# Kernel optimization log

Hardware: AMD Instinct MI355X
Metric: run time of the kernel (lower is better)

## Reference

```python
import jax, jax.numpy as jnp
import numpy as np

SEQ, BATCH, INP = 20, 16384, 2
HID, EMB = 256, 64
TARGET_LEN = 30


def setup_inputs() -> dict:
    key = jax.random.key(0)
    ks = jax.random.split(key, 12)
    s = 0.1
    return {
        "x_input": jax.random.normal(ks[0], (SEQ, BATCH, INP), dtype=jnp.float32),
        # encoder embedding Linear(input_size -> emb_dim)
        "W_emb": jax.random.normal(ks[1], (EMB, INP), dtype=jnp.float32) * s,
        "b_emb": jax.random.normal(ks[2], (EMB,), dtype=jnp.float32) * s,
        # encoder LSTM (input EMB -> hidden HID), PyTorch gate order i,f,g,o; bias = b_ih + b_hh
        "W_ih_enc": jax.random.normal(ks[3], (4 * HID, EMB), dtype=jnp.float32) * s,
        "W_hh_enc": jax.random.normal(ks[4], (4 * HID, HID), dtype=jnp.float32) * s,
        "b_enc": jax.random.normal(ks[5], (4 * HID,), dtype=jnp.float32) * s,
        # decoder LSTM (input INP -> hidden HID)
        "W_ih_dec": jax.random.normal(ks[6], (4 * HID, INP), dtype=jnp.float32) * s,
        "W_hh_dec": jax.random.normal(ks[7], (4 * HID, HID), dtype=jnp.float32) * s,
        "b_dec": jax.random.normal(ks[8], (4 * HID,), dtype=jnp.float32) * s,
        # decoder output Linear(hidden -> input_size)
        "W_out": jax.random.normal(ks[9], (INP, HID), dtype=jnp.float32) * s,
        "b_out": jax.random.normal(ks[10], (INP,), dtype=jnp.float32) * s,
        "target_len": TARGET_LEN,
    }


def _lstm_cell(x, h, c, W_ih, W_hh, b):
    # x: [B, in], h/c: [B, H]; PyTorch gate order: input, forget, cell(g), output
    gates = x @ W_ih.T + h @ W_hh.T + b  # [B, 4H]
    i, f, g, o = jnp.split(gates, 4, axis=-1)
    c_new = jax.nn.sigmoid(f) * c + jax.nn.sigmoid(i) * jnp.tanh(g)
    h_new = jax.nn.sigmoid(o) * jnp.tanh(c_new)
    return h_new, c_new


def reference(x_input, W_emb, b_emb, W_ih_enc, W_hh_enc, b_enc,
              W_ih_dec, W_hh_dec, b_dec, W_out, b_out, target_len):
    B = x_input.shape[1]
    # --- encoder ---
    x_emb = x_input @ W_emb.T + b_emb  # [S, B, EMB]
    h0 = jnp.zeros((B, HID), dtype=x_input.dtype)
    c0 = jnp.zeros((B, HID), dtype=x_input.dtype)

    def enc_step(carry, xt):
        h, c = carry
        h, c = _lstm_cell(xt, h, c, W_ih_enc, W_hh_enc, b_enc)
        return (h, c), None

    (h_enc, c_enc), _ = jax.lax.scan(enc_step, (h0, c0), x_emb)

    dec_in0 = x_input[-1]  # [B, INP]

    def dec_step(carry, _):
        di, h, c = carry
        h, c = _lstm_cell(di, h, c, W_ih_dec, W_hh_dec, b_dec)
        out = h @ W_out.T + b_out  # [B, INP]
        return (out, h, c), out

    _, outputs = jax.lax.scan(dec_step, (dec_in0, h_enc, c_enc), None,
                              length=int(target_len))
    return outputs  # [target_len, B, INP]
```

## Files before the change

kernel.cpp:

```cpp
#include <hip/hip_runtime.h>


#define SEQ  20
#define TLEN 30
#define LOG2E  1.442695041f
#define LOG2E2 2.885390082f

typedef _Float16 half8   __attribute__((ext_vector_type(8)));
typedef _Float16 half4   __attribute__((ext_vector_type(4)));
typedef _Float16 half2v  __attribute__((ext_vector_type(2)));
typedef float    floatx4 __attribute__((ext_vector_type(4)));

__device__ _Float16 g_w_enc[1024 * 288];
__device__ _Float16 g_w_dec0[1024 * 288];
__device__ _Float16 g_w_deff[1024 * 288];
__device__ _Float16 g_wout[512];

__global__ void prep_kernel(const float* __restrict__ W_emb,
                            const float* __restrict__ b_emb,
                            const float* __restrict__ W_ih_enc,
                            const float* __restrict__ W_hh_enc,
                            const float* __restrict__ b_enc,
                            const float* __restrict__ W_ih_dec,
                            const float* __restrict__ W_hh_dec,
                            const float* __restrict__ b_dec,
                            const float* __restrict__ W_out,
                            const float* __restrict__ b_out) {
    int gid = blockIdx.x * blockDim.x + threadIdx.x;
    int stride = gridDim.x * blockDim.x;
    for (int s = gid; s < 1024 * 288; s += stride) {
        int n = s / 288, k = s - n * 288;
        int g = n >> 8, c = (n >> 4) & 15, l16 = n & 15;
        int w = c >> 1, cc = c & 1;
        int i = cc * 4 + g;
        int kt = k >> 5, q = (k >> 3) & 3, j = k & 7;
        int dst = ((w * 9 + kt) * 8 + i) * 512 + q * 128 + l16 * 8 + j;
        float sc = (g == 2) ? LOG2E2 : LOG2E;
        float fe = 0.f, fd = 0.f, ff = 0.f;
        if (k < 256) {
            fe = W_hh_enc[n * 256 + k];
            fd = W_hh_dec[n * 256 + k];
            ff = fd + W_ih_dec[2 * n] * W_out[k]
                    + W_ih_dec[2 * n + 1] * W_out[256 + k];
        } else {
            int kp = k - 256;
            if (kp < 2) {
                fd = W_ih_dec[2 * n + kp];
                const float* wr = &W_ih_enc[n * 64];
                for (int e = 0; e < 64; e++) fe = fmaf(wr[e], W_emb[2 * e + kp], fe);
            } else if (kp == 2) {
                fd = b_dec[n];
                ff = b_dec[n] + W_ih_dec[2 * n] * b_out[0]
                              + W_ih_dec[2 * n + 1] * b_out[1];
                fe = b_enc[n];
                const float* wr = &W_ih_enc[n * 64];
                for (int e = 0; e < 64; e++) fe = fmaf(wr[e], b_emb[e], fe);
            }
        }
        g_w_enc[dst]  = (_Float16)(fe * sc);
        g_w_dec0[dst] = (_Float16)(fd * sc);
        g_w_deff[dst] = (_Float16)(ff * sc);
    }
    if (gid < 512) g_wout[gid] = (_Float16)W_out[gid];
}

__global__ __launch_bounds__(512, 2) void lstm_fused(
        const float* __restrict__ x_input,
        const float* __restrict__ b_out,
        float* __restrict__ out)
{
    __shared__ __align__(16) _Float16 h_pack[2][18432];
    __shared__ __align__(16) float    partial_lds[2][8 * 132];
    __shared__ int flag_lds[9];
    __shared__ int cnt_lds[2];

    const int tid = threadIdx.x;
    const int w   = tid >> 6;
    const int L   = tid & 63;
    const int l16 = L & 15;
    const int q   = L >> 4;
    const long row0 = (long)blockIdx.x * 64;

    {
        int* hz = (int*)&h_pack[0][0];
        for (int idx = tid; idx < 18432; idx += 512) hz[idx] = 0;
        if (tid < 9) flag_lds[tid] = 0;
        if (tid < 2) cnt_lds[tid] = 0;
    }
    __syncthreads();
    if (tid < 128) {
        int buf = tid >> 6, b = tid & 63;
        h_pack[buf][((b >> 4) * 9 + 8) * 512 + (b & 15) * 8 + 2] = (_Float16)1.f;
    }
    if (tid < 128) {
        int b = tid >> 1, jj = tid & 1;
        h_pack[0][((b >> 4) * 9 + 8) * 512 + (b & 15) * 8 + jj] =
            (_Float16)x_input[(row0 + b) * 2 + jj];
    }

    const float2 bo2 = make_float2(b_out[0], b_out[1]);
    const int aoff = q * 128 + l16 * 8;
    const _Float16* __restrict__ wenc_w  = &g_w_enc[w * 36864];
    const _Float16* __restrict__ wdec0_w = &g_w_dec0[w * 36864];
    const _Float16* __restrict__ wdeff_w = &g_w_deff[w * 36864];

    _Float16 wo[2][2][4];
#pragma unroll
    for (int jj = 0; jj < 2; jj++)
#pragma unroll
        for (int cc = 0; cc < 2; cc++)
#pragma unroll
            for (int r = 0; r < 4; r++)
                wo[jj][cc][r] = g_wout[jj * 256 + 32 * w + 16 * cc + 4 * q + r];

    floatx4 acc[8][4];
    float   c_st[4][2][4];
#pragma unroll
    for (int nt = 0; nt < 4; nt++)
#pragma unroll
        for (int cc = 0; cc < 2; cc++)
#pragma unroll
            for (int r = 0; r < 4; r++) c_st[nt][cc][r] = 0.f;

    __syncthreads();

    auto flag_ld = [&](int idx) {
        return __hip_atomic_load(&flag_lds[idx], __ATOMIC_RELAXED,
                                 __HIP_MEMORY_SCOPE_WORKGROUP);
    };

#pragma unroll 1
    for (int t = 0; t < SEQ + TLEN; t++) {
        const _Float16* __restrict__ Wb =
            (t < SEQ) ? wenc_w : (t == SEQ) ? wdec0_w : wdeff_w;
        const _Float16* __restrict__ hp = h_pack[t & 1];
        _Float16* __restrict__ hn = h_pack[(t + 1) & 1];

        int pf = flag_ld(0);
#pragma unroll
        for (int kt = 0; kt < 9; kt++) {
            int pfn = 0;
            if (kt < 8) pfn = flag_ld(kt + 1);
            while (pf < t) {
                __builtin_amdgcn_s_sleep(1);
                pf = flag_ld(kt);
            }
            __builtin_amdgcn_sched_barrier(0);
            half8 B[4];
#pragma unroll
            for (int nt = 0; nt < 4; nt++)
                B[nt] = *(const half8*)&hp[(nt * 9 + kt) * 512 + aoff];
#pragma unroll
            for (int i = 0; i < 8; i++) {
                half8 Aw = *(const half8*)&Wb[(kt * 8 + i) * 512 + aoff];
                if (kt == 0) {
#pragma unroll
                    for (int nt = 0; nt < 4; nt++)
                        acc[i][nt] = __builtin_amdgcn_mfma_f32_16x16x32_f16(
                            Aw, B[nt], (floatx4)(0.f), 0, 0, 0);
                } else {
#pragma unroll
                    for (int nt = 0; nt < 4; nt++)
                        acc[i][nt] = __builtin_amdgcn_mfma_f32_16x16x32_f16(
                            Aw, B[nt], acc[i][nt], 0, 0, 0);
                }
            }
            pf = pfn;
        }

        float2 xv2 = make_float2(0.f, 0.f);
        if (w == 0 && t < SEQ) {
            int srct = (t + 1 < SEQ) ? t + 1 : SEQ - 1;
            xv2 = *(const float2*)&x_input[(long)srct * 32768 + (row0 + L) * 2];
        }

        const bool dec = (t >= SEQ);
        const int par = t & 1;
        float po[4][2];
#pragma unroll
        for (int nt = 0; nt < 4; nt++) { po[nt][0] = 0.f; po[nt][1] = 0.f; }

#pragma unroll
        for (int nt = 0; nt < 4; nt++)
#pragma unroll
            for (int cc = 0; cc < 2; cc++) {
                half4 hv4;
                float hvf[4];
#pragma unroll
                for (int r = 0; r < 4; r++) {
                    float ai = acc[cc * 4 + 0][nt][r];
                    float af = acc[cc * 4 + 1][nt][r];
                    float ag = acc[cc * 4 + 2][nt][r];
                    float ao = acc[cc * 4 + 3][nt][r];
                    float eI = __builtin_amdgcn_exp2f(-ai);
                    float eG = __builtin_amdgcn_exp2f(-ag);
                    float eF = __builtin_amdgcn_exp2f(-af);
                    float eO = __builtin_amdgcn_exp2f(-ao);
                    float ig = (1.f - eG) *
                        __builtin_amdgcn_rcpf((1.f + eI) * (1.f + eG));
                    float fs = __builtin_amdgcn_rcpf(1.f + eF);
                    float cn = fmaf(fs, c_st[nt][cc][r], ig);
                    c_st[nt][cc][r] = cn;
                    float cnc = fminf(fmaxf(cn, -12.f), 12.f);
                    float eC = __builtin_amdgcn_exp2f(-LOG2E2 * cnc);
                    float hv = (1.f - eC) *
                        __builtin_amdgcn_rcpf((1.f + eO) * (1.f + eC));
                    hvf[r] = hv;
                    hv4[r] = (_Float16)hv;
                }
                *(half4*)&hn[(nt * 9 + w) * 512 + (2 * cc + (q >> 1)) * 128 +
                             l16 * 8 + 4 * (q & 1)] = hv4;
                if (dec) {
#pragma unroll
                    for (int r = 0; r < 4; r++) {
                        po[nt][0] = fmaf(hvf[r], (float)wo[0][cc][r], po[nt][0]);
                        po[nt][1] = fmaf(hvf[r], (float)wo[1][cc][r], po[nt][1]);
                    }
                }
            }

        if (L == 0)
            __hip_atomic_store(&flag_lds[w], t + 1, __ATOMIC_RELEASE,
                               __HIP_MEMORY_SCOPE_WORKGROUP);

        if (w == 0) {
            if (t < SEQ) {
                half2v xh; xh[0] = (_Float16)xv2.x; xh[1] = (_Float16)xv2.y;
                *(half2v*)&hn[((L >> 4) * 9 + 8) * 512 + (L & 15) * 8] = xh;
            }
            if (L == 0)
                __hip_atomic_store(&flag_lds[8], t + 1, __ATOMIC_RELEASE,
                                   __HIP_MEMORY_SCOPE_WORKGROUP);
        }

        if (dec) {
#pragma unroll
            for (int nt = 0; nt < 4; nt++)
#pragma unroll
                for (int jj = 0; jj < 2; jj++) {
                    float s = po[nt][jj];
                    s += __shfl_xor(s, 16);
                    s += __shfl_xor(s, 32);
                    po[nt][jj] = s;
                }
            if (q == 0) {
                float* pl = &partial_lds[par][w * 132];
#pragma unroll
                for (int nt = 0; nt < 4; nt++) {
                    pl[nt * 16 + l16]      = po[nt][0];
                    pl[66 + nt * 16 + l16] = po[nt][1];
                }
            }
            __threadfence_block();
            int arr = 0;
            if (L == 0) arr = atomicAdd(&cnt_lds[par], 1);
            arr = __shfl(arr, 0);
            if (arr == 7) {
                if (L == 0)
                    __hip_atomic_store(&cnt_lds[par], 0, __ATOMIC_RELAXED,
                                       __HIP_MEMORY_SCOPE_WORKGROUP);
                float s0 = bo2.x, s1 = bo2.y;
#pragma unroll
                for (int w8 = 0; w8 < 8; w8++) {
                    s0 += partial_lds[par][w8 * 132 + L];
                    s1 += partial_lds[par][w8 * 132 + 66 + L];
                }
                *(float2*)&out[(long)(t - SEQ) * 32768 + (row0 + L) * 2] =
                    make_float2(s0, s1);
            }
        }
    }
}

extern "C" void kernel_launch(void* const* d_in, const int* in_sizes, int n_in,
                              void* d_out, int out_size, void* d_ws, size_t ws_size,
                              hipStream_t stream) {
    (void)in_sizes; (void)n_in; (void)d_ws; (void)ws_size; (void)out_size;
    const float* x      = (const float*)d_in[0];
    const float* W_emb  = (const float*)d_in[1];
    const float* b_emb  = (const float*)d_in[2];
    const float* W_ih_e = (const float*)d_in[3];
    const float* W_hh_e = (const float*)d_in[4];
    const float* b_enc  = (const float*)d_in[5];
    const float* W_ih_d = (const float*)d_in[6];
    const float* W_hh_d = (const float*)d_in[7];
    const float* b_dec  = (const float*)d_in[8];
    const float* W_out  = (const float*)d_in[9];
    const float* b_out  = (const float*)d_in[10];
    float* outp = (float*)d_out;

    prep_kernel<<<512, 256, 0, stream>>>(W_emb, b_emb, W_ih_e, W_hh_e, b_enc,
                                         W_ih_d, W_hh_d, b_dec, W_out, b_out);
    lstm_fused<<<256, 512, 0, stream>>>(x, b_out, outp);
}
```

Measured before the change: 614.2 us.

## Split workgroup into two batch-half groups with paired-wave weight sharing

Rebuilds the work split so that each of two 4-wave groups handles 32 batch rows and each wave computes 64 hidden units (16 gate tiles × 2 batch tiles), where before each wave did 32 hidden units for all 64 rows. Sync changes from per-k-tile flags to per-group hidden-state flags, plus an 'amf' handshake that staggers the two groups so that waves with the same weight slice run in lockstep, presumably to share weight loads through cache. The aim is to cut cross-wave dependency and increase weight reuse per B load. In exchange each wave streams twice as many weight fragments per step, and the new spin-wait coupling adds latency and some deadlock risk.

```diff
diff --git a/kernel.cpp b/kernel.cpp
--- a/kernel.cpp
+++ b/kernel.cpp
@@ -31,10 +31,10 @@
     for (int s = gid; s < 1024 * 288; s += stride) {
         int n = s / 288, k = s - n * 288;
         int g = n >> 8, c = (n >> 4) & 15, l16 = n & 15;
-        int w = c >> 1, cc = c & 1;
+        int wl = c >> 2, cc = c & 3;
         int i = cc * 4 + g;
         int kt = k >> 5, q = (k >> 3) & 3, j = k & 7;
-        int dst = ((w * 9 + kt) * 8 + i) * 512 + q * 128 + l16 * 8 + j;
+        int dst = ((wl * 9 + kt) * 16 + i) * 512 + q * 128 + l16 * 8 + j;
         float sc = (g == 2) ? LOG2E2 : LOG2E;
         float fe = 0.f, fd = 0.f, ff = 0.f;
         if (k < 256) {
@@ -70,12 +70,16 @@
         float* __restrict__ out)
 {
     __shared__ __align__(16) _Float16 h_pack[2][18432];
-    __shared__ __align__(16) float    partial_lds[2][8 * 132];
-    __shared__ int flag_lds[9];
-    __shared__ int cnt_lds[2];
+    __shared__ __align__(16) float    partial_lds[2][2][4 * 68];
+    __shared__ int hflag[2][4];
+    __shared__ int amf[2][4];
+    __shared__ int cnt[2][2];
 
     const int tid = threadIdx.x;
     const int w   = tid >> 6;
+    const int grp = w >> 2;
+    const int wl  = w & 3;
+    const int ntb = grp * 2;
     const int L   = tid & 63;
     const int l16 = L & 15;
     const int q   = L >> 4;
@@ -84,8 +88,9 @@
     {
         int* hz = (int*)&h_pack[0][0];
         for (int idx = tid; idx < 18432; idx += 512) hz[idx] = 0;
-        if (tid < 9) flag_lds[tid] = 0;
-        if (tid < 2) cnt_lds[tid] = 0;
+        if (tid < 8)  hflag[tid >> 2][tid & 3] = 0;
+        if (tid < 16 && tid >= 8) amf[(tid - 8) >> 2][tid & 3] = 0;
+        if (tid < 20 && tid >= 16) cnt[(tid - 16) >> 1][tid & 1] = 0;
     }
     __syncthreads();
     if (tid < 128) {
@@ -98,34 +103,34 @@
             (_Float16)x_input[(row0 + b) * 2 + jj];
     }
 
-    const float2 bo2 = make_float2(b_out[0], b_out[1]);
+    const float boL = b_out[L & 1];
     const int aoff = q * 128 + l16 * 8;
-    const _Float16* __restrict__ wenc_w  = &g_w_enc[w * 36864];
-    const _Float16* __restrict__ wdec0_w = &g_w_dec0[w * 36864];
-    const _Float16* __restrict__ wdeff_w = &g_w_deff[w * 36864];
-
-    _Float16 wo[2][2][4];
+    const _Float16* __restrict__ wenc_w  = &g_w_enc[wl * 73728];
+    const _Float16* __restrict__ wdec0_w = &g_w_dec0[wl * 73728];
+    const _Float16* __restrict__ wdeff_w = &g_w_deff[wl * 73728];
+
+    _Float16 wo[2][4][4];
 #pragma unroll
     for (int jj = 0; jj < 2; jj++)
 #pragma unroll
-        for (int cc = 0; cc < 2; cc++)
+        for (int cc = 0; cc < 4; cc++)
 #pragma unroll
             for (int r = 0; r < 4; r++)
-                wo[jj][cc][r] = g_wout[jj * 256 + 32 * w + 16 * cc + 4 * q + r];
-
-    floatx4 acc[8][4];
-    float   c_st[4][2][4];
-#pragma unroll
-    for (int nt = 0; nt < 4; nt++)
-#pragma unroll
-        for (int cc = 0; cc < 2; cc++)
-#pragma unroll
-            for (int r = 0; r < 4; r++) c_st[nt][cc][r] = 0.f;
+                wo[jj][cc][r] = g_wout[jj * 256 + 64 * wl + 16 * cc + 4 * q + r];
+
+    floatx4 acc[16][2];
+    float   c_st[2][4][4];
+#pragma unroll
+    for (int ntl = 0; ntl < 2; ntl++)
+#pragma unroll
+        for (int cc = 0; cc < 4; cc++)
+#pragma unroll
+            for (int r = 0; r < 4; r++) c_st[ntl][cc][r] = 0.f;
 
     __syncthreads();
 
-    auto flag_ld = [&](int idx) {
-        return __hip_atomic_load(&flag_lds[idx], __ATOMIC_RELAXED,
+    auto ld32 = [&](int* p) {
+        return __hip_atomic_load(p, __ATOMIC_RELAXED,
                                  __HIP_MEMORY_SCOPE_WORKGROUP);
     };
 
@@ -136,62 +141,65 @@
         const _Float16* __restrict__ hp = h_pack[t & 1];
         _Float16* __restrict__ hn = h_pack[(t + 1) & 1];
 
-        int pf = flag_ld(0);
+        if (grp == 1) {
+            while (ld32(&amf[0][wl]) < t + 1) __builtin_amdgcn_s_sleep(1);
+        } else {
+            while (ld32(&amf[1][wl]) < t - 1) __builtin_amdgcn_s_sleep(1);
+        }
+        while (ld32(&hflag[grp][0]) < t || ld32(&hflag[grp][1]) < t ||
+               ld32(&hflag[grp][2]) < t || ld32(&hflag[grp][3]) < t)
+            __builtin_amdgcn_s_sleep(1);
+        __builtin_amdgcn_sched_barrier(0);
+
 #pragma unroll
         for (int kt = 0; kt < 9; kt++) {
-            int pfn = 0;
-            if (kt < 8) pfn = flag_ld(kt + 1);
-            while (pf < t) {
-                __builtin_amdgcn_s_sleep(1);
-                pf = flag_ld(kt);
-            }
-            __builtin_amdgcn_sched_barrier(0);
-            half8 B[4];
-#pragma unroll
-            for (int nt = 0; nt < 4; nt++)
-                B[nt] = *(const half8*)&hp[(nt * 9 + kt) * 512 + aoff];
-#pragma unroll
-            for (int i = 0; i < 8; i++) {
-                half8 Aw = *(const half8*)&Wb[(kt * 8 + i) * 512 + aoff];
+            half8 B0 = *(const half8*)&hp[(ntb * 9 + kt) * 512 + aoff];
+            half8 B1 = *(const half8*)&hp[((ntb + 1) * 9 + kt) * 512 + aoff];
+#pragma unroll
+            for (int i = 0; i < 16; i++) {
+                half8 Aw = *(const half8*)&Wb[(kt * 16 + i) * 512 + aoff];
                 if (kt == 0) {
-#pragma unroll
-                    for (int nt = 0; nt < 4; nt++)
-                        acc[i][nt] = __builtin_amdgcn_mfma_f32_16x16x32_f16(
-                            Aw, B[nt], (floatx4)(0.f), 0, 0, 0);
+                    acc[i][0] = __builtin_amdgcn_mfma_f32_16x16x32_f16(
+                        Aw, B0, (floatx4)(0.f), 0, 0, 0);
+                    acc[i][1] = __builtin_amdgcn_mfma_f32_16x16x32_f16(
+                        Aw, B1, (floatx4)(0.f), 0, 0, 0);
                 } else {
-#pragma unroll
-                    for (int nt = 0; nt < 4; nt++)
-                        acc[i][nt] = __builtin_amdgcn_mfma_f32_16x16x32_f16(
-                            Aw, B[nt], acc[i][nt], 0, 0, 0);
-                }
-            }
-            pf = pfn;
-        }
+                    acc[i][0] = __builtin_amdgcn_mfma_f32_16x16x32_f16(
+                        Aw, B0, acc[i][0], 0, 0, 0);
+                    acc[i][1] = __builtin_amdgcn_mfma_f32_16x16x32_f16(
+                        Aw, B1, acc[i][1], 0, 0, 0);
+                }
+            }
+        }
+
+        if (L == 0)
+            __hip_atomic_store(&amf[grp][wl], t + 1, __ATOMIC_RELAXED,
+                               __HIP_MEMORY_SCOPE_WORKGROUP);
 
         float2 xv2 = make_float2(0.f, 0.f);
-        if (w == 0 && t < SEQ) {
+        if (wl == 0 && t < SEQ && L < 32) {
             int srct = (t + 1 < SEQ) ? t + 1 : SEQ - 1;
-            xv2 = *(const float2*)&x_input[(long)srct * 32768 + (row0 + L) * 2];
+            xv2 = *(const float2*)
+                &x_input[(long)srct * 32768 + (row0 + grp * 32 + L) * 2];
         }
 
         const bool dec = (t >= SEQ);
         const int par = t & 1;
-        float po[4][2];
-#pragma unroll
-        for (int nt = 0; nt < 4; nt++) { po[nt][0] = 0.f; po[nt][1] = 0.f; }
-
-#pragma unroll
-        for (int nt = 0; nt < 4; nt++)
-#pragma unroll
-            for (int cc = 0; cc < 2; cc++) {
+        float po[2][2];
+        po[0][0] = 0.f; po[0][1] = 0.f; po[1][0] = 0.f; po[1][1] = 0.f;
+
+#pragma unroll
+        for (int ntl = 0; ntl < 2; ntl++)
+#pragma unroll
+            for (int cc = 0; cc < 4; cc++) {
                 half4 hv4;
                 float hvf[4];
 #pragma unroll
                 for (int r = 0; r < 4; r++) {
-                    float ai = acc[cc * 4 + 0][nt][r];
-                    float af = acc[cc * 4 + 1][nt][r];
-                    float ag = acc[cc * 4 + 2][nt][r];
-                    float ao = acc[cc * 4 + 3][nt][r];
+                    float ai = acc[cc * 4 + 0][ntl][r];
+                    float af = acc[cc * 4 + 1][ntl][r];
+                    float ag = acc[cc * 4 + 2][ntl][r];
+                    float ao = acc[cc * 4 + 3][ntl][r];
                     float eI = __builtin_amdgcn_exp2f(-ai);
                     float eG = __builtin_amdgcn_exp2f(-ag);
                     float eF = __builtin_amdgcn_exp2f(-af);
@@ -199,8 +207,8 @@
                     float ig = (1.f - eG) *
                         __builtin_amdgcn_rcpf((1.f + eI) * (1.f + eG));
                     float fs = __builtin_amdgcn_rcpf(1.f + eF);
-                    float cn = fmaf(fs, c_st[nt][cc][r], ig);
-                    c_st[nt][cc][r] = cn;
+                    float cn = fmaf(fs, c_st[ntl][cc][r], ig);
+                    c_st[ntl][cc][r] = cn;
                     float cnc = fminf(fmaxf(cn, -12.f), 12.f);
                     float eC = __builtin_amdgcn_exp2f(-LOG2E2 * cnc);
                     float hv = (1.f - eC) *
@@ -208,65 +216,60 @@
                     hvf[r] = hv;
                     hv4[r] = (_Float16)hv;
                 }
-                *(half4*)&hn[(nt * 9 + w) * 512 + (2 * cc + (q >> 1)) * 128 +
+                *(half4*)&hn[((ntb + ntl) * 9 + 2 * wl + (cc >> 1)) * 512 +
+                             (2 * (cc & 1) + (q >> 1)) * 128 +
                              l16 * 8 + 4 * (q & 1)] = hv4;
                 if (dec) {
 #pragma unroll
                     for (int r = 0; r < 4; r++) {
-                        po[nt][0] = fmaf(hvf[r], (float)wo[0][cc][r], po[nt][0]);
-                        po[nt][1] = fmaf(hvf[r], (float)wo[1][cc][r], po[nt][1]);
+                        po[ntl][0] = fmaf(hvf[r], (float)wo[0][cc][r], po[ntl][0]);
+                        po[ntl][1] = fmaf(hvf[r], (float)wo[1][cc][r], po[ntl][1]);
                     }
                 }
             }
 
+        if (wl == 0 && t < SEQ && L < 32) {
+            int b = grp * 32 + L;
+            half2v xh; xh[0] = (_Float16)xv2.x; xh[1] = (_Float16)xv2.y;
+            *(half2v*)&hn[((b >> 4) * 9 + 8) * 512 + (b & 15) * 8] = xh;
+        }
+
         if (L == 0)
-            __hip_atomic_store(&flag_lds[w], t + 1, __ATOMIC_RELEASE,
+            __hip_atomic_store(&hflag[grp][wl], t + 1, __ATOMIC_RELEASE,
                                __HIP_MEMORY_SCOPE_WORKGROUP);
 
-        if (w == 0) {
-            if (t < SEQ) {
-                half2v xh; xh[0] = (_Float16)xv2.x; xh[1] = (_Float16)xv2.y;
-                *(half2v*)&hn[((L >> 4) * 9 + 8) * 512 + (L & 15) * 8] = xh;
-            }
-            if (L == 0)
-                __hip_atomic_store(&flag_lds[8], t + 1, __ATOMIC_RELEASE,
-                                   __HIP_MEMORY_SCOPE_WORKGROUP);
-        }
-
         if (dec) {
 #pragma unroll
-            for (int nt = 0; nt < 4; nt++)
+            for (int ntl = 0; ntl < 2; ntl++)
 #pragma unroll
                 for (int jj = 0; jj < 2; jj++) {
-                    float s = po[nt][jj];
+                    float s = po[ntl][jj];
                     s += __shfl_xor(s, 16);
                     s += __shfl_xor(s, 32);
-                    po[nt][jj] = s;
+                    po[ntl][jj] = s;
                 }
             if (q == 0) {
-                float* pl = &partial_lds[par][w * 132];
-#pragma unroll
-                for (int nt = 0; nt < 4; nt++) {
-                    pl[nt * 16 + l16]      = po[nt][0];
-                    pl[66 + nt * 16 + l16] = po[nt][1];
+                float* pl = &partial_lds[grp][par][wl * 68];
+#pragma unroll
+                for (int ntl = 0; ntl < 2; ntl++) {
+                    pl[ntl * 16 + l16]      = po[ntl][0];
+                    pl[34 + ntl * 16 + l16] = po[ntl][1];
                 }
             }
             __threadfence_block();
             int arr = 0;
-            if (L == 0) arr = atomicAdd(&cnt_lds[par], 1);
+            if (L == 0) arr = atomicAdd(&cnt[grp][par], 1);
             arr = __shfl(arr, 0);
-            if (arr == 7) {
+            if (arr == 3) {
                 if (L == 0)
-                    __hip_atomic_store(&cnt_lds[par], 0, __ATOMIC_RELAXED,
+                    __hip_atomic_store(&cnt[grp][par], 0, __ATOMIC_RELAXED,
                                        __HIP_MEMORY_SCOPE_WORKGROUP);
-                float s0 = bo2.x, s1 = bo2.y;
-#pragma unroll
-                for (int w8 = 0; w8 < 8; w8++) {
-                    s0 += partial_lds[par][w8 * 132 + L];
-                    s1 += partial_lds[par][w8 * 132 + 66 + L];
-                }
-                *(float2*)&out[(long)(t - SEQ) * 32768 + (row0 + L) * 2] =
-                    make_float2(s0, s1);
+                int r = L >> 1, jj = L & 1;
+                float s = boL;
+                const float* pl = &partial_lds[grp][par][jj * 34 + r];
+#pragma unroll
+                for (int w4 = 0; w4 < 4; w4++) s += pl[w4 * 68];
+                out[(long)(t - SEQ) * 32768 + (row0 + grp * 32 + r) * 2 + jj] = s;
             }
         }
     }
```

Result: slower. 1.100 ms (+79.1%).

## Split LSTM waves into MFMA producers and elementwise consumers via LDS gate ring

Applied to the files above, without the earlier changes.

Warp-specializes the fused LSTM block. Four waves compute gate GEMM tiles with MFMA and write fp16 gate values into a double-buffered LDS ring. Four other waves consume them to apply the sigmoid/tanh cell update, write h, and handle the output projection. The weight layout is reshuffled so each producer wave owns four quarter-tiles, and the k-tile order is permuted to match when h chunks become ready. The aim is to overlap transcendental math with matrix work. In exchange, gate pre-activations are rounded to fp16, LDS traffic and spin-wait handshakes increase, and only half the waves issue MFMAs.

```diff
diff --git a/kernel.cpp b/kernel.cpp
--- a/kernel.cpp
+++ b/kernel.cpp
@@ -30,11 +30,11 @@
     int stride = gridDim.x * blockDim.x;
     for (int s = gid; s < 1024 * 288; s += stride) {
         int n = s / 288, k = s - n * 288;
-        int g = n >> 8, c = (n >> 4) & 15, l16 = n & 15;
-        int w = c >> 1, cc = c & 1;
-        int i = cc * 4 + g;
-        int kt = k >> 5, q = (k >> 3) & 3, j = k & 7;
-        int dst = ((w * 9 + kt) * 8 + i) * 512 + q * 128 + l16 * 8 + j;
+        int g = n >> 8, rem = n & 255, l16 = n & 15;
+        int pw = rem >> 6, r = (rem >> 5) & 1, u = (rem >> 4) & 1;
+        int qi = 2 * r + u;
+        int kt = k >> 5, q = (k >> 3) & 3, j8 = k & 7;
+        int dst = (((pw * 4 + qi) * 9 + kt) * 4 + g) * 512 + q * 128 + l16 * 8 + j8;
         float sc = (g == 2) ? LOG2E2 : LOG2E;
         float fe = 0.f, fd = 0.f, ff = 0.f;
         if (k < 256) {
@@ -70,9 +70,12 @@
         float* __restrict__ out)
 {
     __shared__ __align__(16) _Float16 h_pack[2][18432];
-    __shared__ __align__(16) float    partial_lds[2][8 * 132];
-    __shared__ int flag_lds[9];
-    __shared__ int cnt_lds[2];
+    __shared__ __align__(16) _Float16 gates_ring[2][4][4352];
+    __shared__ __align__(16) float    partial_lds[2][4 * 136];
+    __shared__ int hf[9];
+    __shared__ int gprod[4];
+    __shared__ int gcons[4];
+    __shared__ int cnt[2];
 
     const int tid = threadIdx.x;
     const int w   = tid >> 6;
@@ -80,12 +83,16 @@
     const int l16 = L & 15;
     const int q   = L >> 4;
     const long row0 = (long)blockIdx.x * 64;
+    const int aoff = q * 128 + l16 * 8;
+    const int lb   = q * 68 + l16 * 4;
 
     {
         int* hz = (int*)&h_pack[0][0];
         for (int idx = tid; idx < 18432; idx += 512) hz[idx] = 0;
-        if (tid < 9) flag_lds[tid] = 0;
-        if (tid < 2) cnt_lds[tid] = 0;
+        if (tid < 9) hf[tid] = 0;
+        if (tid >= 16 && tid < 20) gprod[tid - 16] = 0;
+        if (tid >= 32 && tid < 36) gcons[tid - 32] = 0;
+        if (tid >= 48 && tid < 50) cnt[tid - 48] = 0;
     }
     __syncthreads();
     if (tid < 128) {
@@ -94,179 +101,235 @@
     }
     if (tid < 128) {
         int b = tid >> 1, jj = tid & 1;
-        h_pack[0][((b >> 4) * 9 + 8) * 512 + (b & 15) * 8 + jj] =
+        h_pack[1][((b >> 4) * 9 + 8) * 512 + (b & 15) * 8 + jj] =
             (_Float16)x_input[(row0 + b) * 2 + jj];
     }
-
-    const float2 bo2 = make_float2(b_out[0], b_out[1]);
-    const int aoff = q * 128 + l16 * 8;
-    const _Float16* __restrict__ wenc_w  = &g_w_enc[w * 36864];
-    const _Float16* __restrict__ wdec0_w = &g_w_dec0[w * 36864];
-    const _Float16* __restrict__ wdeff_w = &g_w_deff[w * 36864];
-
-    _Float16 wo[2][2][4];
-#pragma unroll
-    for (int jj = 0; jj < 2; jj++)
-#pragma unroll
-        for (int cc = 0; cc < 2; cc++)
-#pragma unroll
-            for (int r = 0; r < 4; r++)
-                wo[jj][cc][r] = g_wout[jj * 256 + 32 * w + 16 * cc + 4 * q + r];
-
-    floatx4 acc[8][4];
-    float   c_st[4][2][4];
-#pragma unroll
-    for (int nt = 0; nt < 4; nt++)
-#pragma unroll
-        for (int cc = 0; cc < 2; cc++)
-#pragma unroll
-            for (int r = 0; r < 4; r++) c_st[nt][cc][r] = 0.f;
-
     __syncthreads();
 
-    auto flag_ld = [&](int idx) {
-        return __hip_atomic_load(&flag_lds[idx], __ATOMIC_RELAXED,
-                                 __HIP_MEMORY_SCOPE_WORKGROUP);
+    auto ldacq = [&](int* p) {
+        return __hip_atomic_load(p, __ATOMIC_ACQUIRE, __HIP_MEMORY_SCOPE_WORKGROUP);
     };
-
+    auto strel = [&](int* p, int v) {
+        if (L == 0)
+            __hip_atomic_store(p, v, __ATOMIC_RELEASE, __HIP_MEMORY_SCOPE_WORKGROUP);
+    };
+
+    if (w < 4) {
+        constexpr int ord9[9] = {0, 2, 4, 6, 1, 3, 5, 7, 8};
 #pragma unroll 1
-    for (int t = 0; t < SEQ + TLEN; t++) {
-        const _Float16* __restrict__ Wb =
-            (t < SEQ) ? wenc_w : (t == SEQ) ? wdec0_w : wdeff_w;
-        const _Float16* __restrict__ hp = h_pack[t & 1];
-        _Float16* __restrict__ hn = h_pack[(t + 1) & 1];
-
-        int pf = flag_ld(0);
-#pragma unroll
-        for (int kt = 0; kt < 9; kt++) {
-            int pfn = 0;
-            if (kt < 8) pfn = flag_ld(kt + 1);
-            while (pf < t) {
-                __builtin_amdgcn_s_sleep(1);
-                pf = flag_ld(kt);
-            }
-            __builtin_amdgcn_sched_barrier(0);
-            half8 B[4];
+        for (int t = 0; t < SEQ + TLEN; t++) {
+            const _Float16* __restrict__ Wt =
+                ((t < SEQ) ? g_w_enc : (t == SEQ) ? g_w_dec0 : g_w_deff)
+                + w * 73728;
+            const _Float16* __restrict__ hp = h_pack[(t + 1) & 1];
+#pragma unroll 1
+            for (int qi = 0; qi < 4; qi++) {
+                const _Float16* __restrict__ Wq = Wt + qi * 18432;
+                floatx4 acc[4][4];
+                if (qi == 0) {
+                    int pf = ldacq(&hf[0]);
+#pragma unroll
+                    for (int idx = 0; idx < 9; idx++) {
+                        int kt = ord9[idx];
+                        int pfn = 0;
+                        if (idx < 8) pfn = ldacq(&hf[ord9[idx + 1]]);
+                        while (pf < t) {
+                            __builtin_amdgcn_s_sleep(1);
+                            pf = ldacq(&hf[kt]);
+                        }
+                        __builtin_amdgcn_sched_barrier(0);
+                        half8 B[4];
+#pragma unroll
+                        for (int nt = 0; nt < 4; nt++)
+                            B[nt] = *(const half8*)&hp[(nt * 9 + kt) * 512 + aoff];
+#pragma unroll
+                        for (int g = 0; g < 4; g++) {
+                            half8 Aw = *(const half8*)&Wq[(kt * 4 + g) * 512 + aoff];
+                            if (kt == 0) {
+#pragma unroll
+                                for (int nt = 0; nt < 4; nt++)
+                                    acc[g][nt] = __builtin_amdgcn_mfma_f32_16x16x32_f16(
+                                        Aw, B[nt], (floatx4)(0.f), 0, 0, 0);
+                            } else {
+#pragma unroll
+                                for (int nt = 0; nt < 4; nt++)
+                                    acc[g][nt] = __builtin_amdgcn_mfma_f32_16x16x32_f16(
+                                        Aw, B[nt], acc[g][nt], 0, 0, 0);
+                            }
+                        }
+                        pf = pfn;
+                    }
+                } else {
+#pragma unroll
+                    for (int kt = 0; kt < 9; kt++) {
+                        half8 B[4];
+#pragma unroll
+                        for (int nt = 0; nt < 4; nt++)
+                            B[nt] = *(const half8*)&hp[(nt * 9 + kt) * 512 + aoff];
+#pragma unroll
+                        for (int g = 0; g < 4; g++) {
+                            half8 Aw = *(const half8*)&Wq[(kt * 4 + g) * 512 + aoff];
+                            if (kt == 0) {
+#pragma unroll
+                                for (int nt = 0; nt < 4; nt++)
+                                    acc[g][nt] = __builtin_amdgcn_mfma_f32_16x16x32_f16(
+                                        Aw, B[nt], (floatx4)(0.f), 0, 0, 0);
+                            } else {
+#pragma unroll
+                                for (int nt = 0; nt < 4; nt++)
+                                    acc[g][nt] = __builtin_amdgcn_mfma_f32_16x16x32_f16(
+                                        Aw, B[nt], acc[g][nt], 0, 0, 0);
+                            }
+                        }
+                    }
+                }
+                const int seq = 4 * t + qi;
+                while (ldacq(&gcons[w]) < seq - 1) __builtin_amdgcn_s_sleep(1);
+                __builtin_amdgcn_sched_barrier(0);
+                _Float16* gc = &gates_ring[seq & 1][w][0];
+#pragma unroll
+                for (int g = 0; g < 4; g++)
+#pragma unroll
+                    for (int nt = 0; nt < 4; nt++) {
+                        half4 hv;
+#pragma unroll
+                        for (int r4 = 0; r4 < 4; r4++)
+                            hv[r4] = (_Float16)acc[g][nt][r4];
+                        *(half4*)&gc[(g * 4 + nt) * 272 + lb] = hv;
+                    }
+                strel(&gprod[w], seq + 1);
+            }
+        }
+    } else {
+        const int e = w - 4;
+        const float2 bo2 = make_float2(b_out[0], b_out[1]);
+        float wo_reg[4][4][2];
+#pragma unroll
+        for (int qi = 0; qi < 4; qi++)
+#pragma unroll
+            for (int r4 = 0; r4 < 4; r4++) {
+                int c = 64 * e + 32 * (qi >> 1) + 16 * (qi & 1) + 4 * q + r4;
+                wo_reg[qi][r4][0] = (float)g_wout[c];
+                wo_reg[qi][r4][1] = (float)g_wout[256 + c];
+            }
+        float c_st[4][4][4];
+#pragma unroll
+        for (int qi = 0; qi < 4; qi++)
 #pragma unroll
             for (int nt = 0; nt < 4; nt++)
-                B[nt] = *(const half8*)&hp[(nt * 9 + kt) * 512 + aoff];
-#pragma unroll
-            for (int i = 0; i < 8; i++) {
-                half8 Aw = *(const half8*)&Wb[(kt * 8 + i) * 512 + aoff];
-                if (kt == 0) {
+#pragma unroll
+                for (int r4 = 0; r4 < 4; r4++) c_st[qi][nt][r4] = 0.f;
+
+#pragma unroll 1
+        for (int t = 0; t < SEQ + TLEN; t++) {
+            const int par = t & 1;
+            _Float16* __restrict__ hn = h_pack[par];
+            const bool dec = (t >= SEQ);
+            float po[4][2];
+#pragma unroll
+            for (int nt = 0; nt < 4; nt++) { po[nt][0] = 0.f; po[nt][1] = 0.f; }
+
+#pragma unroll 1
+            for (int qi = 0; qi < 4; qi++) {
+                const int seq = 4 * t + qi;
+                const int r = qi >> 1, u = qi & 1;
+                while (ldacq(&gprod[e]) < seq + 1) __builtin_amdgcn_s_sleep(1);
+                __builtin_amdgcn_sched_barrier(0);
+                const _Float16* gc = &gates_ring[seq & 1][e][0];
+                half4 gh[4][4];
+#pragma unroll
+                for (int g = 0; g < 4; g++)
 #pragma unroll
                     for (int nt = 0; nt < 4; nt++)
-                        acc[i][nt] = __builtin_amdgcn_mfma_f32_16x16x32_f16(
-                            Aw, B[nt], (floatx4)(0.f), 0, 0, 0);
-                } else {
-#pragma unroll
-                    for (int nt = 0; nt < 4; nt++)
-                        acc[i][nt] = __builtin_amdgcn_mfma_f32_16x16x32_f16(
-                            Aw, B[nt], acc[i][nt], 0, 0, 0);
-                }
-            }
-            pf = pfn;
-        }
-
-        float2 xv2 = make_float2(0.f, 0.f);
-        if (w == 0 && t < SEQ) {
-            int srct = (t + 1 < SEQ) ? t + 1 : SEQ - 1;
-            xv2 = *(const float2*)&x_input[(long)srct * 32768 + (row0 + L) * 2];
-        }
-
-        const bool dec = (t >= SEQ);
-        const int par = t & 1;
-        float po[4][2];
-#pragma unroll
-        for (int nt = 0; nt < 4; nt++) { po[nt][0] = 0.f; po[nt][1] = 0.f; }
-
-#pragma unroll
-        for (int nt = 0; nt < 4; nt++)
-#pragma unroll
-            for (int cc = 0; cc < 2; cc++) {
-                half4 hv4;
-                float hvf[4];
-#pragma unroll
-                for (int r = 0; r < 4; r++) {
-                    float ai = acc[cc * 4 + 0][nt][r];
-                    float af = acc[cc * 4 + 1][nt][r];
-                    float ag = acc[cc * 4 + 2][nt][r];
-                    float ao = acc[cc * 4 + 3][nt][r];
-                    float eI = __builtin_amdgcn_exp2f(-ai);
-                    float eG = __builtin_amdgcn_exp2f(-ag);
-                    float eF = __builtin_amdgcn_exp2f(-af);
-                    float eO = __builtin_amdgcn_exp2f(-ao);
-                    float ig = (1.f - eG) *
-                        __builtin_amdgcn_rcpf((1.f + eI) * (1.f + eG));
-                    float fs = __builtin_amdgcn_rcpf(1.f + eF);
-                    float cn = fmaf(fs, c_st[nt][cc][r], ig);
-                    c_st[nt][cc][r] = cn;
-                    float cnc = fminf(fmaxf(cn, -12.f), 12.f);
-                    float eC = __builtin_amdgcn_exp2f(-LOG2E2 * cnc);
-                    float hv = (1.f - eC) *
-                        __builtin_amdgcn_rcpf((1.f + eO) * (1.f + eC));
-                    hvf[r] = hv;
-                    hv4[r] = (_Float16)hv;
-                }
-                *(half4*)&hn[(nt * 9 + w) * 512 + (2 * cc + (q >> 1)) * 128 +
-                             l16 * 8 + 4 * (q & 1)] = hv4;
-                if (dec) {
-#pragma unroll
-                    for (int r = 0; r < 4; r++) {
-                        po[nt][0] = fmaf(hvf[r], (float)wo[0][cc][r], po[nt][0]);
-                        po[nt][1] = fmaf(hvf[r], (float)wo[1][cc][r], po[nt][1]);
-                    }
-                }
-            }
-
-        if (L == 0)
-            __hip_atomic_store(&flag_lds[w], t + 1, __ATOMIC_RELEASE,
-                               __HIP_MEMORY_SCOPE_WORKGROUP);
-
-        if (w == 0) {
-            if (t < SEQ) {
-                half2v xh; xh[0] = (_Float16)xv2.x; xh[1] = (_Float16)xv2.y;
-                *(half2v*)&hn[((L >> 4) * 9 + 8) * 512 + (L & 15) * 8] = xh;
-            }
-            if (L == 0)
-                __hip_atomic_store(&flag_lds[8], t + 1, __ATOMIC_RELEASE,
-                                   __HIP_MEMORY_SCOPE_WORKGROUP);
-        }
-
-        if (dec) {
-#pragma unroll
-            for (int nt = 0; nt < 4; nt++)
-#pragma unroll
-                for (int jj = 0; jj < 2; jj++) {
-                    float s = po[nt][jj];
-                    s += __shfl_xor(s, 16);
-                    s += __shfl_xor(s, 32);
-                    po[nt][jj] = s;
-                }
-            if (q == 0) {
-                float* pl = &partial_lds[par][w * 132];
+                        gh[g][nt] = *(const half4*)&gc[(g * 4 + nt) * 272 + lb];
 #pragma unroll
                 for (int nt = 0; nt < 4; nt++) {
-                    pl[nt * 16 + l16]      = po[nt][0];
-                    pl[66 + nt * 16 + l16] = po[nt][1];
-                }
-            }
-            __threadfence_block();
-            int arr = 0;
-            if (L == 0) arr = atomicAdd(&cnt_lds[par], 1);
-            arr = __shfl(arr, 0);
-            if (arr == 7) {
-                if (L == 0)
-                    __hip_atomic_store(&cnt_lds[par], 0, __ATOMIC_RELAXED,
-                                       __HIP_MEMORY_SCOPE_WORKGROUP);
-                float s0 = bo2.x, s1 = bo2.y;
-#pragma unroll
-                for (int w8 = 0; w8 < 8; w8++) {
-                    s0 += partial_lds[par][w8 * 132 + L];
-                    s1 += partial_lds[par][w8 * 132 + 66 + L];
-                }
-                *(float2*)&out[(long)(t - SEQ) * 32768 + (row0 + L) * 2] =
-                    make_float2(s0, s1);
+                    half4 hv4;
+                    float hvf[4];
+#pragma unroll
+                    for (int r4 = 0; r4 < 4; r4++) {
+                        float ai = (float)gh[0][nt][r4];
+                        float af = (float)gh[1][nt][r4];
+                        float ag = (float)gh[2][nt][r4];
+                        float ao = (float)gh[3][nt][r4];
+                        float eI = __builtin_amdgcn_exp2f(-ai);
+                        float eG = __builtin_amdgcn_exp2f(-ag);
+                        float eF = __builtin_amdgcn_exp2f(-af);
+                        float eO = __builtin_amdgcn_exp2f(-ao);
+                        float ig = (1.f - eG) *
+                            __builtin_amdgcn_rcpf((1.f + eI) * (1.f + eG));
+                        float fs = __builtin_amdgcn_rcpf(1.f + eF);
+                        float cn = fmaf(fs, c_st[qi][nt][r4], ig);
+                        c_st[qi][nt][r4] = cn;
+                        float cnc = fminf(fmaxf(cn, -12.f), 12.f);
+                        float eC = __builtin_amdgcn_exp2f(-LOG2E2 * cnc);
+                        float hv = (1.f - eC) *
+                            __builtin_amdgcn_rcpf((1.f + eO) * (1.f + eC));
+                        hvf[r4] = hv;
+                        hv4[r4] = (_Float16)hv;
+                    }
+                    *(half4*)&hn[(nt * 9 + 2 * e + r) * 512 +
+                                 (2 * u + (q >> 1)) * 128 + l16 * 8 + 4 * (q & 1)] = hv4;
+                    if (dec) {
+#pragma unroll
+                        for (int r4 = 0; r4 < 4; r4++) {
+                            po[nt][0] = fmaf(hvf[r4], wo_reg[qi][r4][0], po[nt][0]);
+                            po[nt][1] = fmaf(hvf[r4], wo_reg[qi][r4][1], po[nt][1]);
+                        }
+                    }
+                }
+                if (qi == 1) strel(&hf[2 * e], t + 1);
+                else if (qi == 3) strel(&hf[2 * e + 1], t + 1);
+                strel(&gcons[e], seq + 1);
+            }
+
+            if (e == 0) {
+                if (t < SEQ) {
+                    int srct = (t + 1 < SEQ) ? t + 1 : SEQ - 1;
+                    float2 xv = *(const float2*)
+                        &x_input[(long)srct * 32768 + (row0 + L) * 2];
+                    half2v xh; xh[0] = (_Float16)xv.x; xh[1] = (_Float16)xv.y;
+                    *(half2v*)&hn[((L >> 4) * 9 + 8) * 512 + (L & 15) * 8] = xh;
+                }
+                strel(&hf[8], t + 1);
+            }
+
+            if (dec) {
+#pragma unroll
+                for (int nt = 0; nt < 4; nt++)
+#pragma unroll
+                    for (int jj = 0; jj < 2; jj++) {
+                        float s = po[nt][jj];
+                        s += __shfl_xor(s, 16);
+                        s += __shfl_xor(s, 32);
+                        po[nt][jj] = s;
+                    }
+                if (q == 0) {
+                    float* pl = &partial_lds[par][e * 136];
+#pragma unroll
+                    for (int nt = 0; nt < 4; nt++) {
+                        pl[nt * 16 + l16]      = po[nt][0];
+                        pl[68 + nt * 16 + l16] = po[nt][1];
+                    }
+                }
+                __threadfence_block();
+                int arr = 0;
+                if (L == 0) arr = atomicAdd(&cnt[par], 1);
+                arr = __shfl(arr, 0);
+                if (arr == 3) {
+                    if (L == 0)
+                        __hip_atomic_store(&cnt[par], 0, __ATOMIC_RELAXED,
+                                           __HIP_MEMORY_SCOPE_WORKGROUP);
+                    __threadfence_block();
+                    float s0 = bo2.x, s1 = bo2.y;
+#pragma unroll
+                    for (int e4 = 0; e4 < 4; e4++) {
+                        s0 += partial_lds[par][e4 * 136 + L];
+                        s1 += partial_lds[par][e4 * 136 + 68 + L];
+                    }
+                    *(float2*)&out[(long)(t - SEQ) * 32768 + (row0 + L) * 2] =
+                        make_float2(s0, s1);
+                }
             }
         }
     }
```

Result: slower. 831.3 us (+35.3%).
